# Kernel tuning notes

Hardware: AMD Instinct MI355X
Metric: run time of the kernel (lower is better)

Reference implementation:

```python
import jax, jax.numpy as jnp
import numpy as np

B, N, C = 4, 2048, 768
H = 12
D = C // H  # head_dim = 64
SCALE = D ** -0.5


def setup_inputs() -> dict:
    key = jax.random.key(0)
    ks = jax.random.split(key, 9)
    x = jax.random.normal(ks[0], (B, N, C), dtype=jnp.float32)
    k_in = jax.random.normal(ks[1], (B, N, C), dtype=jnp.float32)
    v_in = jax.random.normal(ks[2], (B, N, C), dtype=jnp.float32)
    rel_pos_bias = jax.random.normal(ks[3], (H, N, N), dtype=jnp.float32)
    # learned params (nn.Linear stores weight [out, in]; y = x @ W.T + b)
    s = C ** -0.5
    Wq = jax.random.normal(ks[4], (C, C), dtype=jnp.float32) * s
    Wk = jax.random.normal(ks[5], (C, C), dtype=jnp.float32) * s
    Wv = jax.random.normal(ks[6], (C, C), dtype=jnp.float32) * s
    Wp = jax.random.normal(ks[7], (C, C), dtype=jnp.float32) * s
    bp = jax.random.normal(ks[8], (C,), dtype=jnp.float32) * 0.01
    return {"x": x, "k_in": k_in, "v_in": v_in, "rel_pos_bias": rel_pos_bias,
            "Wq": Wq, "Wk": Wk, "Wv": Wv, "Wp": Wp, "bp": bp}


def reference(x, k_in, v_in, rel_pos_bias, Wq, Wk, Wv, Wp, bp):
    # linear projections (no q/k/v bias since qkv_bias=False)
    q = jnp.einsum('bnc,dc->bnd', x, Wq)      # [B,N,C]
    k = jnp.einsum('bnc,dc->bnd', k_in, Wk)   # [B,Nk,C]
    v = jnp.einsum('bnc,dc->bnd', v_in, Wv)   # [B,Nv,C]
    # split heads -> [B,H,N,D]
    q = q.reshape(B, N, H, D).transpose(0, 2, 1, 3) * SCALE
    k = k.reshape(B, -1, H, D).transpose(0, 2, 1, 3)
    v = v.reshape(B, -1, H, D).transpose(0, 2, 1, 3)
    attn = jnp.einsum('bhnd,bhmd->bhnm', q, k)          # [B,H,N,Nk]
    attn = attn + rel_pos_bias[None]                    # additive rel-pos bias
    attn = jax.nn.softmax(attn, axis=-1)
    out = jnp.einsum('bhnm,bhmd->bhnd', attn, v)        # [B,H,N,D]
    out = out.transpose(0, 2, 1, 3).reshape(B, N, C)
    return jnp.einsum('bnc,dc->bnd', out, Wp) + bp
```

## Files before the change

kernel.cpp:

```cpp
#include <hip/hip_runtime.h>
#include <stdint.h>
#include <stddef.h>

#define B_ 4
#define N_ 2048
#define C_ 768
#define H_ 12
#define M_ (B_ * N_)

typedef __attribute__((ext_vector_type(8))) short bf16x8_t;
typedef __attribute__((ext_vector_type(4))) float f32x4_t;

__device__ __forceinline__ unsigned pack2_bf16(float f0, float f1) {
  unsigned u0 = __builtin_bit_cast(unsigned, f0) + 0x8000u;
  unsigned u1 = __builtin_bit_cast(unsigned, f1) + 0x8000u;
  return __builtin_amdgcn_perm(u1, u0, 0x07060302u);
}

__device__ __forceinline__ short f2bf(float f) {
  unsigned u = __builtin_bit_cast(unsigned, f);
  u = (u + 0x7FFFu + ((u >> 16) & 1u)) >> 16;
  return (short)u;
}
__device__ __forceinline__ short f2bf_fast(float f) {
  return (short)((__builtin_bit_cast(unsigned, f) + 0x8000u) >> 16);
}

__device__ __forceinline__ void gload_lds16(const short* g, const short* l) {
  __builtin_amdgcn_global_load_lds(
      (const __attribute__((address_space(1))) void*)g,
      (__attribute__((address_space(3))) void*)l, 16, 0, 0);
}

#define XV 1572864
#define WV 147456
__global__ __launch_bounds__(256) void cvt_all(
    const float* __restrict__ x, const float* __restrict__ kin, const float* __restrict__ vin,
    const float* __restrict__ wq, const float* __restrict__ wk, const float* __restrict__ wv,
    const float* __restrict__ wp,
    unsigned short* __restrict__ xb, unsigned short* __restrict__ kb, unsigned short* __restrict__ vb,
    unsigned short* __restrict__ wqb, unsigned short* __restrict__ wkb, unsigned short* __restrict__ wvb,
    unsigned short* __restrict__ wpb)
{
  int i = blockIdx.x * 256 + threadIdx.x;
  const float* s; unsigned short* d; int off;
  if      (i < XV)            { s = x;   d = xb;  off = i; }
  else if (i < 2 * XV)        { s = kin; d = kb;  off = i - XV; }
  else if (i < 3 * XV)        { s = vin; d = vb;  off = i - 2 * XV; }
  else if (i < 3 * XV + WV)   { s = wq;  d = wqb; off = i - 3 * XV; }
  else if (i < 3 * XV + 2*WV) { s = wk;  d = wkb; off = i - 3 * XV - WV; }
  else if (i < 3 * XV + 3*WV) { s = wv;  d = wvb; off = i - 3 * XV - 2 * WV; }
  else                        { s = wp;  d = wpb; off = i - 3 * XV - 3 * WV; }
  float4 v = ((const float4*)s)[off];
  uint2 p;
  p.x = pack2_bf16(v.x, v.y);
  p.y = pack2_bf16(v.z, v.w);
  ((uint2*)d)[off] = p;
}

__global__ __launch_bounds__(256) void proj_qkv(
    const short* __restrict__ xb, const short* __restrict__ kb, const short* __restrict__ vb,
    const short* __restrict__ wqb, const short* __restrict__ wkb, const short* __restrict__ wvb,
    short* __restrict__ q_ws, short* __restrict__ k_ws, short* __restrict__ vt_ws)
{
  const int z = blockIdx.z;
  const short* A = (z == 0) ? xb : (z == 1) ? kb : vb;
  const short* W = (z == 0) ? wqb : (z == 1) ? wkb : wvb;
  const int m0 = blockIdx.x * 128;
  const int n0 = blockIdx.y * 128;

  __shared__ short smem[128 * 136];
  short* As = smem;
  short* Bs = smem + 8192;

  const int t = threadIdx.x;
  const int w = t >> 6, L = t & 63, L15 = L & 15, quad = L >> 4;
  const int wm = w & 1, wn = w >> 1;

  f32x4_t acc[4][4] = {};

  const short* ga = A + (size_t)(m0 + w * 32 + (L >> 3)) * C_ + (L & 7) * 8;
  const short* gb = W + (size_t)(n0 + w * 32 + (L >> 3)) * C_ + (L & 7) * 8;
  const short* la = &As[(w * 32) * 64];
  const short* lb = &Bs[(w * 32) * 64];

  for (int k0 = 0; k0 < C_; k0 += 64) {
    __syncthreads();
    #pragma unroll
    for (int i = 0; i < 4; ++i) {
      gload_lds16(ga + (size_t)i * 8 * C_ + k0, la + i * 512);
      gload_lds16(gb + (size_t)i * 8 * C_ + k0, lb + i * 512);
    }
    __syncthreads();
    #pragma unroll
    for (int kk = 0; kk < 2; ++kk) {
      bf16x8_t af[4], bfr[4];
      #pragma unroll
      for (int mt = 0; mt < 4; ++mt)
        af[mt] = *(const bf16x8_t*)&As[(wm * 64 + mt * 16 + L15) * 64 + kk * 32 + quad * 8];
      #pragma unroll
      for (int nt = 0; nt < 4; ++nt)
        bfr[nt] = *(const bf16x8_t*)&Bs[(wn * 64 + nt * 16 + L15) * 64 + kk * 32 + quad * 8];
      #pragma unroll
      for (int mt = 0; mt < 4; ++mt)
        #pragma unroll
        for (int nt = 0; nt < 4; ++nt)
          acc[mt][nt] = __builtin_amdgcn_mfma_f32_16x16x32_bf16(af[mt], bfr[nt], acc[mt][nt], 0, 0, 0);
    }
  }

  __syncthreads();
  if (z != 2) {
    const float mul = (z == 0) ? 0.125f : 1.0f;
    #pragma unroll
    for (int mt = 0; mt < 4; ++mt)
      #pragma unroll
      for (int nt = 0; nt < 4; ++nt)
        #pragma unroll
        for (int r = 0; r < 4; ++r)
          smem[(wm * 64 + mt * 16 + quad * 4 + r) * 136 + wn * 64 + nt * 16 + L15] =
              f2bf(acc[mt][nt][r] * mul);
  } else {
    #pragma unroll
    for (int nt = 0; nt < 4; ++nt)
      #pragma unroll
      for (int mt = 0; mt < 4; ++mt) {
        uint2 p;
        p.x = pack2_bf16(acc[mt][nt][0], acc[mt][nt][1]);
        p.y = pack2_bf16(acc[mt][nt][2], acc[mt][nt][3]);
        *(uint2*)&smem[(wn * 64 + nt * 16 + L15) * 136 + wm * 64 + mt * 16 + quad * 4] = p;
      }
  }
  __syncthreads();

  short* outp = (z == 0) ? q_ws : (z == 1) ? k_ws : vt_ws;
  const int b = m0 >> 11, nb = m0 & 2047;
  #pragma unroll
  for (int it = 0; it < 8; ++it) {
    const int run = w * 64 + it * 8 + (L >> 3);
    const int row = run >> 1, half = run & 1;
    uint4 val = *(const uint4*)&smem[row * 136 + half * 64 + (L & 7) * 8];
    size_t g;
    if (z != 2) {
      const int h = (n0 >> 6) + half;
      const int m = m0 + row;
      g = (((size_t)((m >> 11) * H_ + h) * N_ + (m & 2047))) * 64 + (L & 7) * 8;
    } else {
      const int c = n0 + row, h = c >> 6, d = c & 63;
      g = ((size_t)(b * H_ + h) * 64 + d) * N_ + nb + half * 64 + (L & 7) * 8;
    }
    *(uint4*)(outp + g) = val;
  }
}

__global__ __launch_bounds__(256) void attn(
    const short* __restrict__ q_ws, const short* __restrict__ k_ws,
    const short* __restrict__ vt_ws, const float* __restrict__ rpb,
    short* __restrict__ attn_out)
{
  const int b = blockIdx.x & 3;
  const int m0 = (blockIdx.x >> 2) * 64;
  const int h = blockIdx.y;
  const int bh = b * H_ + h;

  __shared__ short Qs[64 * 64];
  __shared__ short Ks[64 * 64];
  __shared__ short Vts[80 * 64];
  __shared__ short Ps[4][16 * 72];

  const int t = threadIdx.x;
  const int w = t >> 6, L = t & 63, L15 = L & 15, quad = L >> 4;

  const short* qp  = q_ws  + ((size_t)bh * N_ + m0) * 64;
  const short* kp  = k_ws  + (size_t)bh * N_ * 64;
  const short* vtp = vt_ws + (size_t)bh * 64 * N_;
  const float* bpb = rpb + (size_t)h * N_ * N_;

  #pragma unroll
  for (int i = 0; i < 2; ++i) {
    const int r0 = w * 16 + i * 8;
    gload_lds16(qp + r0 * 64 + L * 8, &Qs[r0 * 64]);
  }
  for (int i = t; i < 16 * 64; i += 256)
    Vts[64 * 64 + i] = (i < 64) ? (short)0x3F80 : (short)0;

  f32x4_t o[5] = {};

  for (int kv0 = 0; kv0 < N_; kv0 += 64) {
    __syncthreads();
    #pragma unroll
    for (int i = 0; i < 2; ++i) {
      const int r0 = w * 16 + i * 8;
      gload_lds16(kp + (size_t)(kv0 + r0) * 64 + L * 8, &Ks[r0 * 64]);
      gload_lds16(vtp + (size_t)(r0 + (L >> 3)) * N_ + kv0 + (L & 7) * 8, &Vts[r0 * 64]);
    }
    float bias[4][4];
    {
      const float* bq = bpb + (size_t)(m0 + w * 16 + quad * 4) * N_ + kv0 + L15;
      #pragma unroll
      for (int r = 0; r < 4; ++r)
        #pragma unroll
        for (int nt = 0; nt < 4; ++nt)
          bias[r][nt] = bq[(size_t)r * N_ + nt * 16];
    }
    __syncthreads();

    bf16x8_t a0 = *(const bf16x8_t*)&Qs[(w * 16 + L15) * 64 + quad * 8];
    bf16x8_t a1 = *(const bf16x8_t*)&Qs[(w * 16 + L15) * 64 + 32 + quad * 8];
    f32x4_t s[4];
    #pragma unroll
    for (int nt = 0; nt < 4; ++nt) {
      f32x4_t sv = {bias[0][nt], bias[1][nt], bias[2][nt], bias[3][nt]};
      bf16x8_t b0 = *(const bf16x8_t*)&Ks[(nt * 16 + L15) * 64 + quad * 8];
      bf16x8_t b1 = *(const bf16x8_t*)&Ks[(nt * 16 + L15) * 64 + 32 + quad * 8];
      sv = __builtin_amdgcn_mfma_f32_16x16x32_bf16(a0, b0, sv, 0, 0, 0);
      s[nt] = __builtin_amdgcn_mfma_f32_16x16x32_bf16(a1, b1, sv, 0, 0, 0);
    }

    #pragma unroll
    for (int nt = 0; nt < 4; ++nt)
      #pragma unroll
      for (int r = 0; r < 4; ++r)
        Ps[w][(quad * 4 + r) * 72 + nt * 16 + L15] = f2bf_fast(__expf(s[nt][r]));

    #pragma unroll
    for (int kk = 0; kk < 2; ++kk) {
      bf16x8_t pa = *(const bf16x8_t*)&Ps[w][L15 * 72 + kk * 32 + quad * 8];
      #pragma unroll
      for (int nt = 0; nt < 5; ++nt) {
        bf16x8_t vb = *(const bf16x8_t*)&Vts[(nt * 16 + L15) * 64 + kk * 32 + quad * 8];
        o[nt] = __builtin_amdgcn_mfma_f32_16x16x32_bf16(pa, vb, o[nt], 0, 0, 0);
      }
    }
  }

  float rl[4];
  #pragma unroll
  for (int r = 0; r < 4; ++r) {
    const float l = __shfl(o[4][r], quad * 16);
    rl[r] = 1.0f / l;
  }
  const int n_base = m0 + w * 16 + quad * 4;
  #pragma unroll
  for (int nt = 0; nt < 4; ++nt) {
    #pragma unroll
    for (int r = 0; r < 4; ++r) {
      const float v = o[nt][r] * rl[r];
      attn_out[((size_t)(b * N_ + n_base + r)) * C_ + h * 64 + nt * 16 + L15] = f2bf(v);
    }
  }
}

__global__ __launch_bounds__(256) void proj_out(
    const short* __restrict__ Abf, const short* __restrict__ wpb,
    const float* __restrict__ bpv, float* __restrict__ out)
{
  const int m0 = blockIdx.x * 128;
  const int n0 = blockIdx.y * 128;

  __shared__ short As[128 * 64];
  __shared__ short Bs[128 * 64];

  const int t = threadIdx.x;
  const int w = t >> 6, L = t & 63, L15 = L & 15, quad = L >> 4;
  const int wm = w & 1, wn = w >> 1;

  f32x4_t acc[4][4] = {};

  const short* ga = Abf + (size_t)(m0 + w * 32 + (L >> 3)) * C_ + (L & 7) * 8;
  const short* gb = wpb + (size_t)(n0 + w * 32 + (L >> 3)) * C_ + (L & 7) * 8;
  const short* la = &As[(w * 32) * 64];
  const short* lb = &Bs[(w * 32) * 64];

  for (int k0 = 0; k0 < C_; k0 += 64) {
    __syncthreads();
    #pragma unroll
    for (int i = 0; i < 4; ++i) {
      gload_lds16(ga + (size_t)i * 8 * C_ + k0, la + i * 512);
      gload_lds16(gb + (size_t)i * 8 * C_ + k0, lb + i * 512);
    }
    __syncthreads();
    #pragma unroll
    for (int kk = 0; kk < 2; ++kk) {
      bf16x8_t af[4], bfr[4];
      #pragma unroll
      for (int mt = 0; mt < 4; ++mt)
        af[mt] = *(const bf16x8_t*)&As[(wm * 64 + mt * 16 + L15) * 64 + kk * 32 + quad * 8];
      #pragma unroll
      for (int nt = 0; nt < 4; ++nt)
        bfr[nt] = *(const bf16x8_t*)&Bs[(wn * 64 + nt * 16 + L15) * 64 + kk * 32 + quad * 8];
      #pragma unroll
      for (int mt = 0; mt < 4; ++mt)
        #pragma unroll
        for (int nt = 0; nt < 4; ++nt)
          acc[mt][nt] = __builtin_amdgcn_mfma_f32_16x16x32_bf16(af[mt], bfr[nt], acc[mt][nt], 0, 0, 0);
    }
  }

  #pragma unroll
  for (int mt = 0; mt < 4; ++mt) {
    const int m_base = m0 + wm * 64 + mt * 16 + quad * 4;
    #pragma unroll
    for (int nt = 0; nt < 4; ++nt) {
      const int c = n0 + wn * 64 + nt * 16 + L15;
      const float bb = bpv[c];
      #pragma unroll
      for (int r = 0; r < 4; ++r)
        out[(size_t)(m_base + r) * C_ + c] = acc[mt][nt][r] + bb;
    }
  }
}

extern "C" void kernel_launch(void* const* d_in, const int* in_sizes, int n_in,
                              void* d_out, int out_size, void* d_ws, size_t ws_size,
                              hipStream_t stream) {
  const float* x    = (const float*)d_in[0];
  const float* k_in = (const float*)d_in[1];
  const float* v_in = (const float*)d_in[2];
  const float* rpb  = (const float*)d_in[3];
  const float* Wq   = (const float*)d_in[4];
  const float* Wk   = (const float*)d_in[5];
  const float* Wv   = (const float*)d_in[6];
  const float* Wp   = (const float*)d_in[7];
  const float* bp   = (const float*)d_in[8];
  float* out = (float*)d_out;

  const size_t SZ = (size_t)B_ * H_ * N_ * 64 * sizeof(short);
  const size_t WSZ = (size_t)C_ * C_ * sizeof(short);
  char* ws = (char*)d_ws;
  short* q_ws  = (short*)(ws);
  short* k_ws  = (short*)(ws + SZ);
  short* vt_ws = (short*)(ws + 2 * SZ);
  short* ao_ws = (short*)(ws + 3 * SZ);
  short* xb    = (short*)(ws + 4 * SZ);
  short* kb    = (short*)(ws + 5 * SZ);
  short* vb    = (short*)(ws + 6 * SZ);
  short* wqb   = (short*)(ws + 7 * SZ);
  short* wkb   = (short*)(ws + 7 * SZ + WSZ);
  short* wvb   = (short*)(ws + 7 * SZ + 2 * WSZ);
  short* wpb   = (short*)(ws + 7 * SZ + 3 * WSZ);

  cvt_all<<<(3 * XV + 4 * WV + 255) / 256, 256, 0, stream>>>(
      x, k_in, v_in, Wq, Wk, Wv, Wp,
      (unsigned short*)xb, (unsigned short*)kb, (unsigned short*)vb,
      (unsigned short*)wqb, (unsigned short*)wkb, (unsigned short*)wvb, (unsigned short*)wpb);
  proj_qkv<<<dim3(M_ / 128, C_ / 128, 3), 256, 0, stream>>>(
      xb, kb, vb, wqb, wkb, wvb, q_ws, k_ws, vt_ws);
  attn<<<dim3(B_ * (N_ / 64), H_), 256, 0, stream>>>(q_ws, k_ws, vt_ws, rpb, ao_ws);
  proj_out<<<dim3(M_ / 128, C_ / 128), 256, 0, stream>>>(ao_ws, wpb, bp, out);
}
```

Before: 532.5 us.

## Stage K/V/bias via register prefetch into padded LDS, keep Q in registers

The attention loop now loads K, V^T and the rel-pos bias tile into registers with 16-byte coalesced global loads before the first barrier, then writes them into padded LDS arrays (stride 72/68) to reduce bank conflicts. The bias tile is read back from LDS in MFMA layout instead of being gathered with strided scalar global loads. Q fragments are loaded straight into registers once, and the P buffer reuses the bias LDS region. This trades direct async global-to-LDS loads for register staging, which raises register pressure and adds LDS traffic. It also relies on aliasing P over bias, which the barriers must order correctly.

```diff
diff --git a/kernel.cpp b/kernel.cpp
--- a/kernel.cpp
+++ b/kernel.cpp
@@ -163,56 +163,63 @@
   const int h = blockIdx.y;
   const int bh = b * H_ + h;
 
-  __shared__ short Qs[64 * 64];
-  __shared__ short Ks[64 * 64];
-  __shared__ short Vts[80 * 64];
-  __shared__ short Ps[4][16 * 72];
+  __shared__ short Ks[64 * 72];
+  __shared__ short Vts[80 * 72];
+  __shared__ float bias_ps[64 * 68];
 
   const int t = threadIdx.x;
   const int w = t >> 6, L = t & 63, L15 = L & 15, quad = L >> 4;
+  const int sr = t >> 2, sc = (t & 3) << 4;
 
   const short* qp  = q_ws  + ((size_t)bh * N_ + m0) * 64;
   const short* kp  = k_ws  + (size_t)bh * N_ * 64;
   const short* vtp = vt_ws + (size_t)bh * 64 * N_;
   const float* bpb = rpb + (size_t)h * N_ * N_;
 
-  #pragma unroll
-  for (int i = 0; i < 2; ++i) {
-    const int r0 = w * 16 + i * 8;
-    gload_lds16(qp + r0 * 64 + L * 8, &Qs[r0 * 64]);
-  }
-  for (int i = t; i < 16 * 64; i += 256)
-    Vts[64 * 64 + i] = (i < 64) ? (short)0x3F80 : (short)0;
+  const bf16x8_t a0 = *(const bf16x8_t*)(qp + (w * 16 + L15) * 64 + quad * 8);
+  const bf16x8_t a1 = *(const bf16x8_t*)(qp + (w * 16 + L15) * 64 + 32 + quad * 8);
+
+  for (int i = t; i < 16 * 72; i += 256) {
+    const int rr = i / 72, cc = i % 72;
+    Vts[(64 + rr) * 72 + cc] = (rr == 0) ? (short)0x3F80 : (short)0;
+  }
+
+  short* Ps_w = (short*)&bias_ps[w * 16 * 68];
 
   f32x4_t o[5] = {};
 
   for (int kv0 = 0; kv0 < N_; kv0 += 64) {
-    __syncthreads();
-    #pragma unroll
-    for (int i = 0; i < 2; ++i) {
-      const int r0 = w * 16 + i * 8;
-      gload_lds16(kp + (size_t)(kv0 + r0) * 64 + L * 8, &Ks[r0 * 64]);
-      gload_lds16(vtp + (size_t)(r0 + (L >> 3)) * N_ + kv0 + (L & 7) * 8, &Vts[r0 * 64]);
-    }
-    float bias[4][4];
+    const short* gk = kp + (size_t)kv0 * 64 + t * 16;
+    uint4 k0r = *(const uint4*)gk;
+    uint4 k1r = *(const uint4*)(gk + 8);
+    const short* gv = vtp + (size_t)sr * N_ + kv0 + sc;
+    uint4 v0r = *(const uint4*)gv;
+    uint4 v1r = *(const uint4*)(gv + 8);
+    float4 br[4];
     {
-      const float* bq = bpb + (size_t)(m0 + w * 16 + quad * 4) * N_ + kv0 + L15;
+      const float* bq = bpb + (size_t)(m0 + sr) * N_ + kv0 + sc;
+      #pragma unroll
+      for (int j = 0; j < 4; ++j) br[j] = *(const float4*)(bq + 4 * j);
+    }
+    __syncthreads();
+    *(uint4*)&Ks[sr * 72 + sc]       = k0r;
+    *(uint4*)&Ks[sr * 72 + sc + 8]   = k1r;
+    *(uint4*)&Vts[sr * 72 + sc]      = v0r;
+    *(uint4*)&Vts[sr * 72 + sc + 8]  = v1r;
+    #pragma unroll
+    for (int j = 0; j < 4; ++j)
+      *(float4*)&bias_ps[sr * 68 + sc + 4 * j] = br[j];
+    __syncthreads();
+
+    f32x4_t s[4];
+    #pragma unroll
+    for (int nt = 0; nt < 4; ++nt) {
+      f32x4_t sv;
       #pragma unroll
       for (int r = 0; r < 4; ++r)
-        #pragma unroll
-        for (int nt = 0; nt < 4; ++nt)
-          bias[r][nt] = bq[(size_t)r * N_ + nt * 16];
-    }
-    __syncthreads();
-
-    bf16x8_t a0 = *(const bf16x8_t*)&Qs[(w * 16 + L15) * 64 + quad * 8];
-    bf16x8_t a1 = *(const bf16x8_t*)&Qs[(w * 16 + L15) * 64 + 32 + quad * 8];
-    f32x4_t s[4];
-    #pragma unroll
-    for (int nt = 0; nt < 4; ++nt) {
-      f32x4_t sv = {bias[0][nt], bias[1][nt], bias[2][nt], bias[3][nt]};
-      bf16x8_t b0 = *(const bf16x8_t*)&Ks[(nt * 16 + L15) * 64 + quad * 8];
-      bf16x8_t b1 = *(const bf16x8_t*)&Ks[(nt * 16 + L15) * 64 + 32 + quad * 8];
+        sv[r] = bias_ps[(w * 16 + quad * 4 + r) * 68 + nt * 16 + L15];
+      bf16x8_t b0 = *(const bf16x8_t*)&Ks[(nt * 16 + L15) * 72 + quad * 8];
+      bf16x8_t b1 = *(const bf16x8_t*)&Ks[(nt * 16 + L15) * 72 + 32 + quad * 8];
       sv = __builtin_amdgcn_mfma_f32_16x16x32_bf16(a0, b0, sv, 0, 0, 0);
       s[nt] = __builtin_amdgcn_mfma_f32_16x16x32_bf16(a1, b1, sv, 0, 0, 0);
     }
@@ -221,14 +228,14 @@
     for (int nt = 0; nt < 4; ++nt)
       #pragma unroll
       for (int r = 0; r < 4; ++r)
-        Ps[w][(quad * 4 + r) * 72 + nt * 16 + L15] = f2bf_fast(__expf(s[nt][r]));
+        Ps_w[(quad * 4 + r) * 72 + nt * 16 + L15] = f2bf_fast(__expf(s[nt][r]));
 
     #pragma unroll
     for (int kk = 0; kk < 2; ++kk) {
-      bf16x8_t pa = *(const bf16x8_t*)&Ps[w][L15 * 72 + kk * 32 + quad * 8];
+      bf16x8_t pa = *(const bf16x8_t*)&Ps_w[L15 * 72 + kk * 32 + quad * 8];
       #pragma unroll
       for (int nt = 0; nt < 5; ++nt) {
-        bf16x8_t vb = *(const bf16x8_t*)&Vts[(nt * 16 + L15) * 64 + kk * 32 + quad * 8];
+        bf16x8_t vb = *(const bf16x8_t*)&Vts[(nt * 16 + L15) * 72 + kk * 32 + quad * 8];
         o[nt] = __builtin_amdgcn_mfma_f32_16x16x32_bf16(pa, vb, o[nt], 0, 0, 0);
       }
     }
```

Result: slower. 838.5 us (+57.5%).
